# Kernel optimization log

Hardware: AMD Instinct MI355X
Metric: run time of the kernel (lower is better)

Reference implementation:

```python
import jax, jax.numpy as jnp
import numpy as np

WS = (4, 4, 4)  # window size
HEADS = 3
HEAD_DIM = 32

def _relative_indices():
    idx = np.array([[x, y, z] for x in range(WS[0]) for y in range(WS[1]) for z in range(WS[2])])
    rel = idx[None, :, :] - idx[:, None, :]  # [T, T, 3]
    rel = rel - rel.min()
    return rel  # values in [0, 2*ws-2]

_REL = _relative_indices()

def setup_inputs() -> dict:
    key = jax.random.key(0)
    k1, k2, k3, k4, k5 = jax.random.split(key, 5)
    dim = 96
    inner = HEADS * HEAD_DIM  # 96
    x = jax.random.normal(k1, (2, 64, 64, 64, dim), dtype=jnp.float32)
    w_qkv = jax.random.normal(k2, (dim, inner * 3), dtype=jnp.float32) * 0.02
    pos_embedding = jax.random.normal(k3, (7, 7, 7), dtype=jnp.float32)
    w_out = jax.random.normal(k4, (inner, dim), dtype=jnp.float32) * 0.02
    b_out = jax.random.normal(k5, (dim,), dtype=jnp.float32) * 0.02
    return {"x": x, "w_qkv": w_qkv, "pos_embedding": pos_embedding,
            "w_out": w_out, "b_out": b_out}

def reference(x, w_qkv, pos_embedding, w_out, b_out):
    b, H, W, D, C = x.shape
    wh, ww, wd = WS
    nwh, nww, nwd = H // wh, W // ww, D // wd
    nw = nwh * nww * nwd
    T = wh * ww * wd  # tokens per window
    scale = HEAD_DIM ** -0.5

    qkv = x @ w_qkv  # [b,H,W,D,3*inner]
    q, k, v = jnp.split(qkv, 3, axis=-1)

    def to_windows(t):
        # [b,H,W,D,h*d] -> [b, h, nw, T, d]
        t = t.reshape(b, nwh, wh, nww, ww, nwd, wd, HEADS, HEAD_DIM)
        t = t.transpose(0, 7, 1, 3, 5, 2, 4, 6, 8)
        return t.reshape(b, HEADS, nw, T, HEAD_DIM)

    q, k, v = map(to_windows, (q, k, v))

    dots = jnp.einsum('bhwid,bhwjd->bhwij', q, k) * scale  # [b,h,nw,T,T]
    bias = pos_embedding[_REL[:, :, 0], _REL[:, :, 1], _REL[:, :, 2]]  # [T,T]
    attn = jax.nn.softmax(dots + bias, axis=-1)
    out = jnp.einsum('bhwij,bhwjd->bhwid', attn, v)  # [b,h,nw,T,d]

    # back to [b,H,W,D,h*d]
    out = out.reshape(b, HEADS, nwh, nww, nwd, wh, ww, wd, HEAD_DIM)
    out = out.transpose(0, 2, 5, 3, 6, 4, 7, 1, 8)
    out = out.reshape(b, H, W, D, HEADS * HEAD_DIM)
    return out @ w_out + b_out
```

## Files before the change

kernel.cpp:

```cpp
#include <hip/hip_runtime.h>


typedef __attribute__((ext_vector_type(8))) short bv8;
typedef __attribute__((ext_vector_type(4))) float fv4;

__device__ __forceinline__ unsigned short f2bf(float f) {
    union { float f; unsigned u; } v; v.f = f;
    unsigned r = v.u + 0x7fffu + ((v.u >> 16) & 1u);
    return (unsigned short)(r >> 16);
}

__device__ __forceinline__ unsigned pack2(float lo, float hi) {
    return (unsigned)f2bf(lo) | ((unsigned)f2bf(hi) << 16);
}

__device__ __forceinline__ bv8 cvt8(const float* __restrict__ p) {
    float4 a = *(const float4*)p;
    float4 b = *(const float4*)(p + 4);
    bv8 r;
    r[0] = (short)f2bf(a.x); r[1] = (short)f2bf(a.y);
    r[2] = (short)f2bf(a.z); r[3] = (short)f2bf(a.w);
    r[4] = (short)f2bf(b.x); r[5] = (short)f2bf(b.y);
    r[6] = (short)f2bf(b.z); r[7] = (short)f2bf(b.w);
    return r;
}

__global__ void prep_kernel(const float* __restrict__ wqkv,
                            const float* __restrict__ wout,
                            const float* __restrict__ pos,
                            float* __restrict__ biasT,
                            unsigned short* __restrict__ wqT,
                            unsigned short* __restrict__ woT)
{
    int id = blockIdx.x * 256 + threadIdx.x;
    if (id < 27648) {
        int n = id / 96, k = id % 96;
        wqT[id] = f2bf(wqkv[k * 288 + n]);
    } else if (id < 36864) {
        int j = id - 27648;
        int n = j / 96, k = j % 96;
        woT[j] = f2bf(wout[k * 96 + n]);
    } else {
        int i = id - 36864;
        int kj = i >> 6, qi = i & 63;
        int dh = ((kj >> 4) & 3) - ((qi >> 4) & 3) + 3;
        int dw = ((kj >> 2) & 3) - ((qi >> 2) & 3) + 3;
        int dd = (kj & 3) - (qi & 3) + 3;
        biasT[kj * 64 + qi] = pos[(dh * 7 + dw) * 7 + dd] * 1.4426950408889634f;
    }
}

__global__ void __launch_bounds__(256, 4) winattn_kernel(
    const float* __restrict__ x,
    const float* __restrict__ b_out,
    const float* __restrict__ biasT,
    const unsigned short* __restrict__ wqT,
    const unsigned short* __restrict__ woT,
    float* __restrict__ out)
{
    __shared__ __align__(16) unsigned short au[4 * 16 * 104];
    __shared__ __align__(16) unsigned short ks[64 * 104];
    __shared__ __align__(16) unsigned short vts[96 * 72];

    const int tid = threadIdx.x;
    const int w = tid >> 6, lane = tid & 63;
    const int c = lane & 15, g = lane >> 4;
    const int widx = blockIdx.x, bb = blockIdx.y;
    const int bh = (widx >> 8) & 15, bw2 = (widx >> 4) & 15, bd = widx & 15;

    const int ST_W = 64 * 96, ST_H = 64 * 64 * 96;
    const int xbase = ((bb * 64 + bh * 4) * 64 + bw2 * 4) * 64 * 96 + bd * 4 * 96;
    const int i0 = w * 16;
    unsigned short* auw = au + w * (16 * 104);

    bv8 af[3];
    {
        int t = i0 + c;
        const float* tp = x + xbase + (t >> 4) * ST_H + ((t >> 2) & 3) * ST_W + (t & 3) * 96;
#pragma unroll
        for (int k = 0; k < 3; ++k)
            af[k] = cvt8(tp + k * 32 + g * 8);
    }

    float brow[4][4];
#pragma unroll
    for (int nt = 0; nt < 4; ++nt)
#pragma unroll
        for (int r = 0; r < 4; ++r)
            brow[nt][r] = biasT[(nt * 16 + 4 * g + r) * 64 + i0 + c];

    const unsigned short* bsrc = wqT + c * 96 + g * 8;
    bv8 b0[3], bn[3];
#pragma unroll
    for (int k = 0; k < 3; ++k) b0[k] = *(const bv8*)(bsrc + k * 32);

#pragma unroll
    for (int nt = 0; nt < 18; ++nt) {
        if (nt < 17) {
#pragma unroll
            for (int k = 0; k < 3; ++k) bn[k] = *(const bv8*)(bsrc + (nt + 1) * 1536 + k * 32);
        }
        fv4 acc = {0.f, 0.f, 0.f, 0.f};
#pragma unroll
        for (int k = 0; k < 3; ++k)
            acc = __builtin_amdgcn_mfma_f32_16x16x32_bf16(af[k], b0[k], acc, 0, 0, 0);
        if (nt < 6) {
#pragma unroll
            for (int r = 0; r < 4; ++r)
                auw[(4 * g + r) * 104 + nt * 16 + c] = f2bf(acc[r]);
        } else if (nt < 12) {
#pragma unroll
            for (int r = 0; r < 4; ++r)
                ks[(i0 + 4 * g + r) * 104 + (nt - 6) * 16 + c] = f2bf(acc[r]);
        } else {
            int d = (nt - 12) * 16 + c;
            *(unsigned*)&vts[d * 72 + i0 + 4 * g]     = pack2(acc[0], acc[1]);
            *(unsigned*)&vts[d * 72 + i0 + 4 * g + 2] = pack2(acc[2], acc[3]);
        }
#pragma unroll
        for (int k = 0; k < 3; ++k) b0[k] = bn[k];
    }
    __syncthreads();

    bv8 qf[3];
#pragma unroll
    for (int h = 0; h < 3; ++h)
        qf[h] = *(const bv8*)&auw[c * 104 + h * 32 + g * 8];

    const float scale2 = 0.17677669529663687f * 1.4426950408889634f;
    const int lsrc0 = (((2 * g) & 3) << 4) + c;
    const int lsrc1 = (((2 * g + 1) & 3) << 4) + c;
    const bool selhi = (g & 2) != 0;

#pragma unroll
    for (int h = 0; h < 3; ++h) {
        bv8 kf[4];
#pragma unroll
        for (int nt = 0; nt < 4; ++nt)
            kf[nt] = *(const bv8*)&ks[(nt * 16 + c) * 104 + h * 32 + g * 8];
        float sv[4][4];
#pragma unroll
        for (int nt = 0; nt < 4; ++nt) {
            fv4 z = {0.f, 0.f, 0.f, 0.f};
            fv4 s = __builtin_amdgcn_mfma_f32_16x16x32_bf16(kf[nt], qf[h], z, 0, 0, 0);
#pragma unroll
            for (int r = 0; r < 4; ++r)
                sv[nt][r] = s[r] * scale2 + brow[nt][r];
        }
        float m01 = fmaxf(fmaxf(sv[0][0], sv[0][1]), fmaxf(sv[0][2], sv[0][3]));
        float m11 = fmaxf(fmaxf(sv[1][0], sv[1][1]), fmaxf(sv[1][2], sv[1][3]));
        float m21 = fmaxf(fmaxf(sv[2][0], sv[2][1]), fmaxf(sv[2][2], sv[2][3]));
        float m31 = fmaxf(fmaxf(sv[3][0], sv[3][1]), fmaxf(sv[3][2], sv[3][3]));
        float mx = fmaxf(fmaxf(m01, m11), fmaxf(m21, m31));
        mx = fmaxf(mx, __shfl_xor(mx, 16, 64));
        mx = fmaxf(mx, __shfl_xor(mx, 32, 64));
        float sm = 0.f;
#pragma unroll
        for (int nt = 0; nt < 4; ++nt)
#pragma unroll
            for (int r = 0; r < 4; ++r) {
                float e = exp2f(sv[nt][r] - mx);
                sv[nt][r] = e;
                sm += e;
            }
        sm += __shfl_xor(sm, 16, 64);
        sm += __shfl_xor(sm, 32, 64);
        float inv = __builtin_amdgcn_rcpf(sm);

        unsigned pk[4][2];
#pragma unroll
        for (int nt = 0; nt < 4; ++nt) {
            pk[nt][0] = pack2(sv[nt][0] * inv, sv[nt][1] * inv);
            pk[nt][1] = pack2(sv[nt][2] * inv, sv[nt][3] * inv);
        }
        bv8 pf[2];
#pragma unroll
        for (int k2 = 0; k2 < 2; ++k2) {
            unsigned w0 = (unsigned)__shfl((int)pk[2 * k2][0],     lsrc0, 64);
            unsigned w1 = (unsigned)__shfl((int)pk[2 * k2][1],     lsrc0, 64);
            unsigned w2 = (unsigned)__shfl((int)pk[2 * k2][0],     lsrc1, 64);
            unsigned w3 = (unsigned)__shfl((int)pk[2 * k2][1],     lsrc1, 64);
            unsigned v0 = (unsigned)__shfl((int)pk[2 * k2 + 1][0], lsrc0, 64);
            unsigned v1 = (unsigned)__shfl((int)pk[2 * k2 + 1][1], lsrc0, 64);
            unsigned v2 = (unsigned)__shfl((int)pk[2 * k2 + 1][0], lsrc1, 64);
            unsigned v3 = (unsigned)__shfl((int)pk[2 * k2 + 1][1], lsrc1, 64);
            unsigned u0 = selhi ? v0 : w0;
            unsigned u1 = selhi ? v1 : w1;
            unsigned u2 = selhi ? v2 : w2;
            unsigned u3 = selhi ? v3 : w3;
            bv8 p;
            p[0] = (short)(u0 & 0xffffu); p[1] = (short)(u0 >> 16);
            p[2] = (short)(u1 & 0xffffu); p[3] = (short)(u1 >> 16);
            p[4] = (short)(u2 & 0xffffu); p[5] = (short)(u2 >> 16);
            p[6] = (short)(u3 & 0xffffu); p[7] = (short)(u3 >> 16);
            pf[k2] = p;
        }
#pragma unroll
        for (int dt = 0; dt < 2; ++dt) {
            fv4 oacc = {0.f, 0.f, 0.f, 0.f};
#pragma unroll
            for (int k2 = 0; k2 < 2; ++k2) {
                bv8 vf = *(const bv8*)&vts[(h * 32 + dt * 16 + c) * 72 + k2 * 32 + g * 8];
                oacc = __builtin_amdgcn_mfma_f32_16x16x32_bf16(pf[k2], vf, oacc, 0, 0, 0);
            }
#pragma unroll
            for (int r = 0; r < 4; ++r)
                auw[(4 * g + r) * 104 + h * 32 + dt * 16 + c] = f2bf(oacc[r]);
        }
    }

    bv8 afo[3];
#pragma unroll
    for (int k = 0; k < 3; ++k)
        afo[k] = *(const bv8*)&auw[c * 104 + k * 32 + g * 8];

    const unsigned short* osrc = woT + c * 96 + g * 8;
    bv8 ob0[3], obn[3];
#pragma unroll
    for (int k = 0; k < 3; ++k) ob0[k] = *(const bv8*)(osrc + k * 32);

#pragma unroll
    for (int nt = 0; nt < 6; ++nt) {
        if (nt < 5) {
#pragma unroll
            for (int k = 0; k < 3; ++k) obn[k] = *(const bv8*)(osrc + (nt + 1) * 1536 + k * 32);
        }
        fv4 acc = {0.f, 0.f, 0.f, 0.f};
#pragma unroll
        for (int k = 0; k < 3; ++k)
            acc = __builtin_amdgcn_mfma_f32_16x16x32_bf16(afo[k], ob0[k], acc, 0, 0, 0);
        int cc = nt * 16 + c;
        float bo = b_out[cc];
#pragma unroll
        for (int r = 0; r < 4; ++r) {
            int t = i0 + 4 * g + r;
            out[xbase + (t >> 4) * ST_H + ((t >> 2) & 3) * ST_W + (t & 3) * 96 + cc] = acc[r] + bo;
        }
#pragma unroll
        for (int k = 0; k < 3; ++k) ob0[k] = obn[k];
    }
}

extern "C" void kernel_launch(void* const* d_in, const int* in_sizes, int n_in,
                              void* d_out, int out_size, void* d_ws, size_t ws_size,
                              hipStream_t stream)
{
    const float* x    = (const float*)d_in[0];
    const float* wqkv = (const float*)d_in[1];
    const float* pos  = (const float*)d_in[2];
    const float* wout = (const float*)d_in[3];
    const float* bout = (const float*)d_in[4];
    float* out = (float*)d_out;

    float* biasT = (float*)d_ws;
    unsigned short* wqT = (unsigned short*)((char*)d_ws + 16384);
    unsigned short* woT = (unsigned short*)((char*)d_ws + 16384 + 55296);

    prep_kernel<<<160, 256, 0, stream>>>(wqkv, wout, pos, biasT, wqT, woT);
    winattn_kernel<<<dim3(4096, 2), 256, 0, stream>>>(x, bout, biasT, wqT, woT, out);
}
```

Measured before the change: 205.2 us.

## Split QKV projection across waves by output tiles instead of token rows

Each wave now loads and converts all 64 window tokens of x and computes a subset of the 18 QKV output column tiles (5/5/4/4 per wave). Before, each wave did its own 16 rows against all 18 tiles. This cuts per-wave weight loads and gives four independent MFMA chains per B fragment, which is meant to improve MFMA throughput and reuse of the weight fragments. The cost is four times more x global loads and bf16 conversions per block, a larger A-fragment register footprint, a runtime loop with an uneven split, and a shared Q buffer indexed by token row.

Result: slower. 220.7 us (+7.6%).

```diff
diff --git a/kernel.cpp b/kernel.cpp
--- a/kernel.cpp
+++ b/kernel.cpp
@@ -58,7 +58,7 @@
     const unsigned short* __restrict__ woT,
     float* __restrict__ out)
 {
-    __shared__ __align__(16) unsigned short au[4 * 16 * 104];
+    __shared__ __align__(16) unsigned short au[64 * 104];
     __shared__ __align__(16) unsigned short ks[64 * 104];
     __shared__ __align__(16) unsigned short vts[96 * 72];
 
@@ -71,16 +71,63 @@
     const int ST_W = 64 * 96, ST_H = 64 * 64 * 96;
     const int xbase = ((bb * 64 + bh * 4) * 64 + bw2 * 4) * 64 * 96 + bd * 4 * 96;
     const int i0 = w * 16;
-    unsigned short* auw = au + w * (16 * 104);
-
-    bv8 af[3];
-    {
-        int t = i0 + c;
-        const float* tp = x + xbase + (t >> 4) * ST_H + ((t >> 2) & 3) * ST_W + (t & 3) * 96;
+
+    bv8 af[4][3];
+#pragma unroll
+    for (int mt = 0; mt < 4; ++mt) {
+        const float* tp = x + xbase + mt * ST_H + ((c >> 2) & 3) * ST_W + (c & 3) * 96;
 #pragma unroll
         for (int k = 0; k < 3; ++k)
-            af[k] = cvt8(tp + k * 32 + g * 8);
-    }
+            af[mt][k] = cvt8(tp + k * 32 + g * 8);
+    }
+
+    const int ntbase = (w < 2) ? w * 5 : 10 + (w - 2) * 4;
+    const int ntcnt  = (w < 2) ? 5 : 4;
+    const unsigned short* bsrc = wqT + c * 96 + g * 8;
+    bv8 b0[3], bn[3];
+#pragma unroll
+    for (int k = 0; k < 3; ++k) b0[k] = *(const bv8*)(bsrc + ntbase * 1536 + k * 32);
+
+    for (int i = 0; i < ntcnt; ++i) {
+        const int nt = ntbase + i;
+        if (i + 1 < ntcnt) {
+#pragma unroll
+            for (int k = 0; k < 3; ++k) bn[k] = *(const bv8*)(bsrc + (nt + 1) * 1536 + k * 32);
+        }
+        fv4 acc[4];
+#pragma unroll
+        for (int mt = 0; mt < 4; ++mt) acc[mt] = (fv4){0.f, 0.f, 0.f, 0.f};
+#pragma unroll
+        for (int k = 0; k < 3; ++k)
+#pragma unroll
+            for (int mt = 0; mt < 4; ++mt)
+                acc[mt] = __builtin_amdgcn_mfma_f32_16x16x32_bf16(af[mt][k], b0[k], acc[mt], 0, 0, 0);
+#pragma unroll
+        for (int mt = 0; mt < 4; ++mt) {
+            int row = mt * 16 + 4 * g;
+            if (nt < 6) {
+#pragma unroll
+                for (int r = 0; r < 4; ++r)
+                    au[(row + r) * 104 + nt * 16 + c] = f2bf(acc[mt][r]);
+            } else if (nt < 12) {
+#pragma unroll
+                for (int r = 0; r < 4; ++r)
+                    ks[(row + r) * 104 + (nt - 6) * 16 + c] = f2bf(acc[mt][r]);
+            } else {
+                int d = (nt - 12) * 16 + c;
+                *(unsigned*)&vts[d * 72 + row]     = pack2(acc[mt][0], acc[mt][1]);
+                *(unsigned*)&vts[d * 72 + row + 2] = pack2(acc[mt][2], acc[mt][3]);
+            }
+        }
+#pragma unroll
+        for (int k = 0; k < 3; ++k) b0[k] = bn[k];
+    }
+    __syncthreads();
+
+    bv8 qf[3];
+#pragma unroll
+    for (int h = 0; h < 3; ++h)
+        qf[h] = *(const bv8*)&au[(i0 + c) * 104 + h * 32 + g * 8];
 
     float brow[4][4];
 #pragma unroll
@@ -88,44 +135,6 @@
 #pragma unroll
         for (int r = 0; r < 4; ++r)
             brow[nt][r] = biasT[(nt * 16 + 4 * g + r) * 64 + i0 + c];
-
-    const unsigned short* bsrc = wqT + c * 96 + g * 8;
-    bv8 b0[3], bn[3];
-#pragma unroll
-    for (int k = 0; k < 3; ++k) b0[k] = *(const bv8*)(bsrc + k * 32);
-
-#pragma unroll
-    for (int nt = 0; nt < 18; ++nt) {
-        if (nt < 17) {
-#pragma unroll
-            for (int k = 0; k < 3; ++k) bn[k] = *(const bv8*)(bsrc + (nt + 1) * 1536 + k * 32);
-        }
-        fv4 acc = {0.f, 0.f, 0.f, 0.f};
-#pragma unroll
-        for (int k = 0; k < 3; ++k)
-            acc = __builtin_amdgcn_mfma_f32_16x16x32_bf16(af[k], b0[k], acc, 0, 0, 0);
-        if (nt < 6) {
-#pragma unroll
-            for (int r = 0; r < 4; ++r)
-                auw[(4 * g + r) * 104 + nt * 16 + c] = f2bf(acc[r]);
-        } else if (nt < 12) {
-#pragma unroll
-            for (int r = 0; r < 4; ++r)
-                ks[(i0 + 4 * g + r) * 104 + (nt - 6) * 16 + c] = f2bf(acc[r]);
-        } else {
-            int d = (nt - 12) * 16 + c;
-            *(unsigned*)&vts[d * 72 + i0 + 4 * g]     = pack2(acc[0], acc[1]);
-            *(unsigned*)&vts[d * 72 + i0 + 4 * g + 2] = pack2(acc[2], acc[3]);
-        }
-#pragma unroll
-        for (int k = 0; k < 3; ++k) b0[k] = bn[k];
-    }
-    __syncthreads();
-
-    bv8 qf[3];
-#pragma unroll
-    for (int h = 0; h < 3; ++h)
-        qf[h] = *(const bv8*)&auw[c * 104 + h * 32 + g * 8];
 
     const float scale2 = 0.17677669529663687f * 1.4426950408889634f;
     const int lsrc0 = (((2 * g) & 3) << 4) + c;
@@ -205,14 +214,14 @@
             }
 #pragma unroll
             for (int r = 0; r < 4; ++r)
-                auw[(4 * g + r) * 104 + h * 32 + dt * 16 + c] = f2bf(oacc[r]);
+                au[(i0 + 4 * g + r) * 104 + h * 32 + dt * 16 + c] = f2bf(oacc[r]);
         }
     }
 
     bv8 afo[3];
 #pragma unroll
     for (int k = 0; k < 3; ++k)
-        afo[k] = *(const bv8*)&auw[c * 104 + k * 32 + g * 8];
+        afo[k] = *(const bv8*)&au[(i0 + c) * 104 + k * 32 + g * 8];
 
     const unsigned short* osrc = woT + c * 96 + g * 8;
     bv8 ob0[3], obn[3];
```

## Keep Q and attention output in registers via lane shuffles instead of LDS

Applied to the files above, without the earlier changes.

Drops the per-wave shared-memory staging buffer for Q and the attention output. Operands are instead computed transposed through swapped MFMA operands and rebuilt into A-fragments with cross-lane shuffles. Softmax normalization moves after the PV product, and the max subtraction is removed entirely. This cuts LDS traffic and shared-memory footprint, and the max-free softmax saves reductions. The cost is more shuffles and a risk of exp overflow if scores are large.

Result: no change. 206.9 us (+0.8%).

```diff
diff --git a/kernel.cpp b/kernel.cpp
--- a/kernel.cpp
+++ b/kernel.cpp
@@ -24,6 +24,25 @@
     r[6] = (short)f2bf(b.z); r[7] = (short)f2bf(b.w);
     return r;
 }
+
+#define REBUILD(dst, lo, hi)  do {                                              \
+    unsigned w0 = (unsigned)__shfl((int)(lo)[0], lsrc0, 64);                    \
+    unsigned w1 = (unsigned)__shfl((int)(lo)[1], lsrc0, 64);                    \
+    unsigned w2 = (unsigned)__shfl((int)(lo)[0], lsrc1, 64);                    \
+    unsigned w3 = (unsigned)__shfl((int)(lo)[1], lsrc1, 64);                    \
+    unsigned v0 = (unsigned)__shfl((int)(hi)[0], lsrc0, 64);                    \
+    unsigned v1 = (unsigned)__shfl((int)(hi)[1], lsrc0, 64);                    \
+    unsigned v2 = (unsigned)__shfl((int)(hi)[0], lsrc1, 64);                    \
+    unsigned v3 = (unsigned)__shfl((int)(hi)[1], lsrc1, 64);                    \
+    unsigned u0 = selhi ? v0 : w0, u1 = selhi ? v1 : w1;                        \
+    unsigned u2 = selhi ? v2 : w2, u3 = selhi ? v3 : w3;                        \
+    bv8 p_;                                                                     \
+    p_[0] = (short)(u0 & 0xffffu); p_[1] = (short)(u0 >> 16);                   \
+    p_[2] = (short)(u1 & 0xffffu); p_[3] = (short)(u1 >> 16);                   \
+    p_[4] = (short)(u2 & 0xffffu); p_[5] = (short)(u2 >> 16);                   \
+    p_[6] = (short)(u3 & 0xffffu); p_[7] = (short)(u3 >> 16);                   \
+    dst = p_;                                                                   \
+} while (0)
 
 __global__ void prep_kernel(const float* __restrict__ wqkv,
                             const float* __restrict__ wout,
@@ -58,7 +77,6 @@
     const unsigned short* __restrict__ woT,
     float* __restrict__ out)
 {
-    __shared__ __align__(16) unsigned short au[4 * 16 * 104];
     __shared__ __align__(16) unsigned short ks[64 * 104];
     __shared__ __align__(16) unsigned short vts[96 * 72];
 
@@ -71,7 +89,10 @@
     const int ST_W = 64 * 96, ST_H = 64 * 64 * 96;
     const int xbase = ((bb * 64 + bh * 4) * 64 + bw2 * 4) * 64 * 96 + bd * 4 * 96;
     const int i0 = w * 16;
-    unsigned short* auw = au + w * (16 * 104);
+
+    const int lsrc0 = (((2 * g) & 3) << 4) + c;
+    const int lsrc1 = (((2 * g + 1) & 3) << 4) + c;
+    const bool selhi = (g & 2) != 0;
 
     bv8 af[3];
     {
@@ -82,18 +103,12 @@
             af[k] = cvt8(tp + k * 32 + g * 8);
     }
 
-    float brow[4][4];
-#pragma unroll
-    for (int nt = 0; nt < 4; ++nt)
-#pragma unroll
-        for (int r = 0; r < 4; ++r)
-            brow[nt][r] = biasT[(nt * 16 + 4 * g + r) * 64 + i0 + c];
-
     const unsigned short* bsrc = wqT + c * 96 + g * 8;
     bv8 b0[3], bn[3];
 #pragma unroll
     for (int k = 0; k < 3; ++k) b0[k] = *(const bv8*)(bsrc + k * 32);
 
+    unsigned pkq[6][2];
 #pragma unroll
     for (int nt = 0; nt < 18; ++nt) {
         if (nt < 17) {
@@ -101,18 +116,23 @@
             for (int k = 0; k < 3; ++k) bn[k] = *(const bv8*)(bsrc + (nt + 1) * 1536 + k * 32);
         }
         fv4 acc = {0.f, 0.f, 0.f, 0.f};
-#pragma unroll
-        for (int k = 0; k < 3; ++k)
-            acc = __builtin_amdgcn_mfma_f32_16x16x32_bf16(af[k], b0[k], acc, 0, 0, 0);
         if (nt < 6) {
 #pragma unroll
-            for (int r = 0; r < 4; ++r)
-                auw[(4 * g + r) * 104 + nt * 16 + c] = f2bf(acc[r]);
+            for (int k = 0; k < 3; ++k)
+                acc = __builtin_amdgcn_mfma_f32_16x16x32_bf16(b0[k], af[k], acc, 0, 0, 0);
+            pkq[nt][0] = pack2(acc[0], acc[1]);
+            pkq[nt][1] = pack2(acc[2], acc[3]);
         } else if (nt < 12) {
+#pragma unroll
+            for (int k = 0; k < 3; ++k)
+                acc = __builtin_amdgcn_mfma_f32_16x16x32_bf16(af[k], b0[k], acc, 0, 0, 0);
 #pragma unroll
             for (int r = 0; r < 4; ++r)
                 ks[(i0 + 4 * g + r) * 104 + (nt - 6) * 16 + c] = f2bf(acc[r]);
         } else {
+#pragma unroll
+            for (int k = 0; k < 3; ++k)
+                acc = __builtin_amdgcn_mfma_f32_16x16x32_bf16(af[k], b0[k], acc, 0, 0, 0);
             int d = (nt - 12) * 16 + c;
             *(unsigned*)&vts[d * 72 + i0 + 4 * g]     = pack2(acc[0], acc[1]);
             *(unsigned*)&vts[d * 72 + i0 + 4 * g + 2] = pack2(acc[2], acc[3]);
@@ -120,17 +140,23 @@
 #pragma unroll
         for (int k = 0; k < 3; ++k) b0[k] = bn[k];
     }
+
+    bv8 qf[3];
+#pragma unroll
+    for (int h = 0; h < 3; ++h)
+        REBUILD(qf[h], pkq[2 * h], pkq[2 * h + 1]);
+
+    float brow[4][4];
+#pragma unroll
+    for (int nt = 0; nt < 4; ++nt)
+#pragma unroll
+        for (int r = 0; r < 4; ++r)
+            brow[nt][r] = biasT[(nt * 16 + 4 * g + r) * 64 + i0 + c];
+
     __syncthreads();
 
-    bv8 qf[3];
-#pragma unroll
-    for (int h = 0; h < 3; ++h)
-        qf[h] = *(const bv8*)&auw[c * 104 + h * 32 + g * 8];
-
     const float scale2 = 0.17677669529663687f * 1.4426950408889634f;
-    const int lsrc0 = (((2 * g) & 3) << 4) + c;
-    const int lsrc1 = (((2 * g + 1) & 3) << 4) + c;
-    const bool selhi = (g & 2) != 0;
+    unsigned pko[6][2];
 
 #pragma unroll
     for (int h = 0; h < 3; ++h) {
@@ -147,19 +173,12 @@
             for (int r = 0; r < 4; ++r)
                 sv[nt][r] = s[r] * scale2 + brow[nt][r];
         }
-        float m01 = fmaxf(fmaxf(sv[0][0], sv[0][1]), fmaxf(sv[0][2], sv[0][3]));
-        float m11 = fmaxf(fmaxf(sv[1][0], sv[1][1]), fmaxf(sv[1][2], sv[1][3]));
-        float m21 = fmaxf(fmaxf(sv[2][0], sv[2][1]), fmaxf(sv[2][2], sv[2][3]));
-        float m31 = fmaxf(fmaxf(sv[3][0], sv[3][1]), fmaxf(sv[3][2], sv[3][3]));
-        float mx = fmaxf(fmaxf(m01, m11), fmaxf(m21, m31));
-        mx = fmaxf(mx, __shfl_xor(mx, 16, 64));
-        mx = fmaxf(mx, __shfl_xor(mx, 32, 64));
         float sm = 0.f;
 #pragma unroll
         for (int nt = 0; nt < 4; ++nt)
 #pragma unroll
             for (int r = 0; r < 4; ++r) {
-                float e = exp2f(sv[nt][r] - mx);
+                float e = exp2f(sv[nt][r]);
                 sv[nt][r] = e;
                 sm += e;
             }
@@ -170,49 +189,31 @@
         unsigned pk[4][2];
 #pragma unroll
         for (int nt = 0; nt < 4; ++nt) {
-            pk[nt][0] = pack2(sv[nt][0] * inv, sv[nt][1] * inv);
-            pk[nt][1] = pack2(sv[nt][2] * inv, sv[nt][3] * inv);
+            pk[nt][0] = pack2(sv[nt][0], sv[nt][1]);
+            pk[nt][1] = pack2(sv[nt][2], sv[nt][3]);
         }
         bv8 pf[2];
 #pragma unroll
-        for (int k2 = 0; k2 < 2; ++k2) {
-            unsigned w0 = (unsigned)__shfl((int)pk[2 * k2][0],     lsrc0, 64);
-            unsigned w1 = (unsigned)__shfl((int)pk[2 * k2][1],     lsrc0, 64);
-            unsigned w2 = (unsigned)__shfl((int)pk[2 * k2][0],     lsrc1, 64);
-            unsigned w3 = (unsigned)__shfl((int)pk[2 * k2][1],     lsrc1, 64);
-            unsigned v0 = (unsigned)__shfl((int)pk[2 * k2 + 1][0], lsrc0, 64);
-            unsigned v1 = (unsigned)__shfl((int)pk[2 * k2 + 1][1], lsrc0, 64);
-            unsigned v2 = (unsigned)__shfl((int)pk[2 * k2 + 1][0], lsrc1, 64);
-            unsigned v3 = (unsigned)__shfl((int)pk[2 * k2 + 1][1], lsrc1, 64);
-            unsigned u0 = selhi ? v0 : w0;
-            unsigned u1 = selhi ? v1 : w1;
-            unsigned u2 = selhi ? v2 : w2;
-            unsigned u3 = selhi ? v3 : w3;
-            bv8 p;
-            p[0] = (short)(u0 & 0xffffu); p[1] = (short)(u0 >> 16);
-            p[2] = (short)(u1 & 0xffffu); p[3] = (short)(u1 >> 16);
-            p[4] = (short)(u2 & 0xffffu); p[5] = (short)(u2 >> 16);
-            p[6] = (short)(u3 & 0xffffu); p[7] = (short)(u3 >> 16);
-            pf[k2] = p;
-        }
+        for (int k2 = 0; k2 < 2; ++k2)
+            REBUILD(pf[k2], pk[2 * k2], pk[2 * k2 + 1]);
+
 #pragma unroll
         for (int dt = 0; dt < 2; ++dt) {
             fv4 oacc = {0.f, 0.f, 0.f, 0.f};
 #pragma unroll
             for (int k2 = 0; k2 < 2; ++k2) {
                 bv8 vf = *(const bv8*)&vts[(h * 32 + dt * 16 + c) * 72 + k2 * 32 + g * 8];
-                oacc = __builtin_amdgcn_mfma_f32_16x16x32_bf16(pf[k2], vf, oacc, 0, 0, 0);
+                oacc = __builtin_amdgcn_mfma_f32_16x16x32_bf16(vf, pf[k2], oacc, 0, 0, 0);
             }
-#pragma unroll
-            for (int r = 0; r < 4; ++r)
-                auw[(4 * g + r) * 104 + h * 32 + dt * 16 + c] = f2bf(oacc[r]);
+            pko[2 * h + dt][0] = pack2(oacc[0] * inv, oacc[1] * inv);
+            pko[2 * h + dt][1] = pack2(oacc[2] * inv, oacc[3] * inv);
         }
     }
 
     bv8 afo[3];
 #pragma unroll
     for (int k = 0; k < 3; ++k)
-        afo[k] = *(const bv8*)&auw[c * 104 + k * 32 + g * 8];
+        REBUILD(afo[k], pko[2 * k], pko[2 * k + 1]);
 
     const unsigned short* osrc = woT + c * 96 + g * 8;
     bv8 ob0[3], obn[3];
```
